# Performance work log

Hardware: AMD Instinct MI355X
Metric: run time of the kernel (lower is better)

## Reference

```python
import jax, jax.numpy as jnp
import numpy as np

EPS = 1e-12  # matches torch F.normalize default eps

def _l2_normalize(v, axis=-1):
    n = jnp.sqrt(jnp.sum(v * v, axis=axis, keepdims=True))
    return v / jnp.maximum(n, EPS)

def setup_inputs() -> dict:
    key = jax.random.key(0)
    k1, k2, k3 = jax.random.split(key, 3)
    B, S, D_IN, D_OUT, T = 4, 4096, 1024, 1024, 1024
    std = 1.0 / np.sqrt(D_IN)
    return {
        "x": jax.random.normal(k1, (B, S, D_IN), dtype=jnp.float32),
        "key_tokens": jax.random.normal(k2, (T, D_IN), dtype=jnp.float32) * std,
        "value_tokens": jax.random.normal(k3, (T, D_OUT), dtype=jnp.float32) * std,
        "temp": jnp.ones((T, 1), dtype=jnp.float32),
    }

def reference(x, key_tokens, value_tokens, temp):
    # x: [B,S,D_in]; key_tokens: [T,D_in]; value_tokens: [T,D_out]; temp: [T,1]
    x_norm = _l2_normalize(x)                      # [B,S,D_in]
    k_norm = _l2_normalize(key_tokens)             # [T,D_in]
    sim = jnp.einsum('bsd,td->bst', x_norm, k_norm)  # [B,S,T]
    sim = sim * jax.nn.sigmoid(temp).reshape(1, 1, -1)
    # mod_softmax: scale each row to RMS-norm sqrt(T), then exact GELU
    T = sim.shape[-1]
    scale = jnp.sqrt(jnp.float32(T)) / jnp.sqrt(jnp.sum(sim * sim, axis=-1, keepdims=True))
    weights = jax.nn.gelu(sim * scale, approximate=False)  # [B,S,T]
    return jnp.einsum('bst,to->bso', weights, value_tokens)  # [B,S,D_out]
```

## Files before the change

### kernel.cpp

```cpp
#include <hip/hip_runtime.h>
#include <math.h>

typedef __attribute__((ext_vector_type(8))) short short8;
typedef __attribute__((ext_vector_type(4))) float floatx4;

__device__ __forceinline__ float bf2f(unsigned short u) {
    union { unsigned int u; float f; } v;
    v.u = ((unsigned int)u) << 16;
    return v.f;
}

__device__ __forceinline__ unsigned short f2bf(float f) {
    union { float f; unsigned int u; } v;
    v.f = f;
    unsigned int r = v.u + 0x7fffu + ((v.u >> 16) & 1u);
    return (unsigned short)(r >> 16);
}

__device__ __forceinline__ void gload16_lds(const void* g, void* l) {
    __builtin_amdgcn_global_load_lds(
        (const __attribute__((address_space(1))) unsigned int*)g,
        (__attribute__((address_space(3))) unsigned int*)l, 16, 0, 0);
}

__device__ __forceinline__ ushort4 cvt4(float4 v, float fa) {
    ushort4 o;
    o.x = f2bf(v.x * fa); o.y = f2bf(v.y * fa);
    o.z = f2bf(v.z * fa); o.w = f2bf(v.w * fa);
    return o;
}

__global__ __launch_bounds__(256) void prep_kernel(
    const float* __restrict__ x, const float* __restrict__ key,
    const float* __restrict__ temp, const float* __restrict__ val,
    unsigned short* __restrict__ xb, unsigned short* __restrict__ kf,
    unsigned short* __restrict__ VT, float* __restrict__ rowsq,
    int M, int T, int D, int Dout, int nRowBlocks) {
    const int bid = blockIdx.x;
    if (bid < nRowBlocks) {
        const int lane = threadIdx.x & 63;
        const int nWaves = nRowBlocks << 2;
        const int totRows = M + T;
        for (int row = (bid << 2) | (int)(threadIdx.x >> 6); row < totRows;
             row += nWaves) {
            const bool isx = row < M;
            const int r = isx ? row : row - M;
            const float4* s4 =
                (const float4*)(isx ? (x + (size_t)r * D) : (key + (size_t)r * D));
            float4 v0 = s4[lane];
            float4 v1 = s4[lane + 64];
            float4 v2 = s4[lane + 128];
            float4 v3 = s4[lane + 192];
            float s = v0.x * v0.x + v0.y * v0.y + v0.z * v0.z + v0.w * v0.w;
            s += v1.x * v1.x + v1.y * v1.y + v1.z * v1.z + v1.w * v1.w;
            s += v2.x * v2.x + v2.y * v2.y + v2.z * v2.z + v2.w * v2.w;
            s += v3.x * v3.x + v3.y * v3.y + v3.z * v3.z + v3.w * v3.w;
#pragma unroll
            for (int o = 32; o > 0; o >>= 1) s += __shfl_xor(s, o, 64);
            float fa = 1.0f / fmaxf(sqrtf(s), 1e-12f);
            if (isx) {
                if (lane == 0) rowsq[r] = 0.0f;
            } else {
                fa = fa / (1.0f + expf(-temp[r]));
            }
            ushort4* dst =
                (ushort4*)(isx ? (xb + (size_t)r * D) : (kf + (size_t)r * D));
            dst[lane] = cvt4(v0, fa);
            dst[lane + 64] = cvt4(v1, fa);
            dst[lane + 128] = cvt4(v2, fa);
            dst[lane + 192] = cvt4(v3, fa);
        }
    } else {
        __shared__ unsigned short tile[64][65];
        const int idx = bid - nRowBlocks;
        const int nCt = Dout >> 6;
        const int c0 = (idx % nCt) * 64;
        const int r0 = (idx / nCt) * 64;
        const int t = threadIdx.x;
        for (int i = t; i < 4096; i += 256) {
            int rr = i >> 6, cc = i & 63;
            tile[rr][cc] = f2bf(val[(size_t)(r0 + rr) * Dout + c0 + cc]);
        }
        __syncthreads();
        for (int i = t; i < 4096; i += 256) {
            int rr = i >> 6, cc = i & 63;
            VT[(size_t)(c0 + rr) * T + r0 + cc] = tile[cc][rr];
        }
    }
}

template <int MODE>
__global__ __launch_bounds__(512, 2) void gemm256(
    const unsigned short* __restrict__ A, const unsigned short* __restrict__ B,
    void* __restrict__ Cv, float* __restrict__ rowsq, int M, int N, int K) {
    __shared__ __align__(16) char smem[131072];
    const int tid = threadIdx.x;
    const int lane = tid & 63;
    const int w = tid >> 6;
    const int wr = w >> 2;
    const int wc = w & 3;
    const int m0 = blockIdx.x * 256;
    const int n0 = blockIdx.y * 256;
    const int q = lane >> 4;
    const int cl = lane & 15;

    const int srow = lane >> 2;
    const int sch = (lane & 3) ^ ((lane & 32) >> 4);
    const unsigned short* gA0 = A + (size_t)(m0 + w * 16 + srow) * K + sch * 8;
    const unsigned short* gA1 = gA0 + (size_t)128 * K;
    const unsigned short* gB0 = B + (size_t)(n0 + w * 16 + srow) * K + sch * 8;
    const unsigned short* gB1 = gB0 + (size_t)128 * K;

    const int LB = (((lane & 15) * 64 + q * 16) ^ ((lane & 8) << 2));

    floatx4 acc[8][4];
#pragma unroll
    for (int i = 0; i < 8; i++)
#pragma unroll
        for (int j = 0; j < 4; j++) acc[i][j] = (floatx4){0.f, 0.f, 0.f, 0.f};

    const int NT = K >> 5;

    auto stage_h = [&](int t, int h) {
        char* base = smem + (size_t)(t & 3) * 32768 + (h * 8 + w) * 1024;
        const size_t ro = (size_t)h * 128 * K;
        const size_t ko = (size_t)t * 32;
        gload16_lds(gA0 + ro + ko, base);
        gload16_lds(gB0 + ro + ko, base + 16384);
    };
    (void)gA1; (void)gB1;

    stage_h(0, 0); stage_h(0, 1);
    stage_h(1, 0); stage_h(1, 1);
    stage_h(2, 0); stage_h(2, 1);
    asm volatile("s_waitcnt vmcnt(8)" ::: "memory");
    __builtin_amdgcn_s_barrier();

    for (int tt = 0; tt < NT; ++tt) {
        const char* sA = smem + (size_t)(tt & 3) * 32768;
        const char* sB = sA + 16384;
        const bool st = (tt + 3) < NT;
        short8 bf[4], af[4];
#pragma unroll
        for (int nt = 0; nt < 4; ++nt)
            bf[nt] = *(const short8*)(sB + (wc * 4 + nt) * 1024 + LB);
#pragma unroll
        for (int mt = 0; mt < 4; ++mt)
            af[mt] = *(const short8*)(sA + (wr * 8 + mt) * 1024 + LB);
        if (st) stage_h(tt + 3, 0);
        __builtin_amdgcn_s_barrier();
        asm volatile("s_waitcnt lgkmcnt(0)" ::: "memory");
        __builtin_amdgcn_s_setprio(1);
#pragma unroll
        for (int mt = 0; mt < 4; ++mt)
#pragma unroll
            for (int nt = 0; nt < 4; ++nt)
                acc[mt][nt] = __builtin_amdgcn_mfma_f32_16x16x32_bf16(
                    af[mt], bf[nt], acc[mt][nt], 0, 0, 0);
        __builtin_amdgcn_s_setprio(0);
        __builtin_amdgcn_s_barrier();
        __builtin_amdgcn_sched_barrier(0);
#pragma unroll
        for (int mt = 0; mt < 4; ++mt)
            af[mt] = *(const short8*)(sA + (wr * 8 + 4 + mt) * 1024 + LB);
        if (st) stage_h(tt + 3, 1);
        if (tt < NT - 3) {
            asm volatile("s_waitcnt vmcnt(8)" ::: "memory");
        } else if (tt == NT - 3) {
            asm volatile("s_waitcnt vmcnt(4)" ::: "memory");
        } else if (tt == NT - 2) {
            asm volatile("s_waitcnt vmcnt(0)" ::: "memory");
        }
        __builtin_amdgcn_s_barrier();
        asm volatile("s_waitcnt lgkmcnt(0)" ::: "memory");
        __builtin_amdgcn_s_setprio(1);
#pragma unroll
        for (int mt = 0; mt < 4; ++mt)
#pragma unroll
            for (int nt = 0; nt < 4; ++nt)
                acc[4 + mt][nt] = __builtin_amdgcn_mfma_f32_16x16x32_bf16(
                    af[mt], bf[nt], acc[4 + mt][nt], 0, 0, 0);
        __builtin_amdgcn_s_setprio(0);
        __builtin_amdgcn_s_barrier();
        __builtin_amdgcn_sched_barrier(0);
    }

#pragma unroll
    for (int mt = 0; mt < 8; ++mt) {
#pragma unroll
        for (int r = 0; r < 4; ++r) {
            const int m = m0 + wr * 128 + mt * 16 + q * 4 + r;
            if (MODE == 0) {
                unsigned short* C = (unsigned short*)Cv;
                float ssq = 0.f;
#pragma unroll
                for (int nt = 0; nt < 4; ++nt) {
                    float v = acc[mt][nt][r];
                    ssq += v * v;
                    C[(size_t)m * N + n0 + wc * 64 + nt * 16 + cl] = f2bf(v);
                }
#pragma unroll
                for (int o = 1; o < 16; o <<= 1) ssq += __shfl_xor(ssq, o, 64);
                if (cl == 0) atomicAdd(&rowsq[m], ssq);
            } else {
                float* C = (float*)Cv;
#pragma unroll
                for (int nt = 0; nt < 4; ++nt)
                    C[(size_t)m * N + n0 + wc * 64 + nt * 16 + cl] =
                        acc[mt][nt][r];
            }
        }
    }
}

__global__ __launch_bounds__(256) void gelu_kernel(unsigned short* __restrict__ sim,
                                                   const float* __restrict__ rowsq,
                                                   int nVec, int t8shift,
                                                   float sqrtT) {
    const int stride = gridDim.x * blockDim.x;
    const float kk = 0.70710678118654752f;
    for (int i = blockIdx.x * blockDim.x + threadIdx.x; i < nVec; i += stride) {
        short8 v = *(const short8*)(sim + (size_t)i * 8);
        const int row = i >> t8shift;
        const float scale = sqrtT / fmaxf(sqrtf(rowsq[row]), 1e-30f);
        short8 o;
#pragma unroll
        for (int j = 0; j < 8; j++) {
            float z = bf2f((unsigned short)v[j]) * scale;
            o[j] = (short)f2bf(0.5f * z * (1.0f + erff(z * kk)));
        }
        *(short8*)(sim + (size_t)i * 8) = o;
    }
}

extern "C" void kernel_launch(void* const* d_in, const int* in_sizes, int n_in,
                              void* d_out, int out_size, void* d_ws, size_t ws_size,
                              hipStream_t stream) {
    const float* x    = (const float*)d_in[0];
    const float* key  = (const float*)d_in[1];
    const float* val  = (const float*)d_in[2];
    const float* temp = (const float*)d_in[3];
    float* out = (float*)d_out;

    const int T = in_sizes[3];
    const int D = in_sizes[1] / T;
    const int Dout = in_sizes[2] / T;
    const int M = in_sizes[0] / D;

    char* ws = (char*)d_ws;
    size_t off = 0;
    unsigned short* xb  = (unsigned short*)(ws + off); off += (size_t)M * D * 2;
    unsigned short* sim = (unsigned short*)(ws + off); off += (size_t)M * T * 2;
    unsigned short* kf  = (unsigned short*)(ws + off); off += (size_t)T * D * 2;
    unsigned short* VT  = (unsigned short*)(ws + off); off += (size_t)Dout * T * 2;
    float* rowsq = (float*)(ws + off); off += (size_t)M * 4;
    (void)ws_size; (void)n_in; (void)out_size;

    const int nTrTiles = (T >> 6) * (Dout >> 6);
    const int nRowBlocks = 1024;
    prep_kernel<<<nRowBlocks + nTrTiles, 256, 0, stream>>>(
        x, key, temp, val, xb, kf, VT, rowsq, M, T, D, Dout, nRowBlocks);
    gemm256<0><<<dim3(M / 256, T / 256), 512, 0, stream>>>(xb, kf, sim, rowsq,
                                                           M, T, D);
    int t8shift = 0;
    {
        int t8 = T >> 3;
        while ((1 << t8shift) < t8) t8shift++;
    }
    gelu_kernel<<<2048, 256, 0, stream>>>(sim, rowsq, M * (T >> 3), t8shift,
                                          sqrtf((float)T));
    gemm256<1><<<dim3(M / 256, Dout / 256), 512, 0, stream>>>(sim, VT, out,
                                                              nullptr, M, Dout, T);
}
```

Baseline: 216.9 us.

## Shrink GEMM tiles to 256x128 with 4 waves and triple-buffered LDS

Both GEMMs switch from a 256x256 tile with 8 waves and a 4-stage LDS ring (128KB) to a 256x128 tile with 4 waves and a 3-stage ring (72KB). This doubles the grid (64x8 blocks) for better CU fill on M=16384 and cuts LDS per block so two blocks fit per CU. The price is lower data reuse per loaded byte, a shallower prefetch depth, and the removal of the sched_barriers, which frees the compiler to reorder around the MFMA phases.

```diff
diff --git a/kernel.cpp b/kernel.cpp
--- a/kernel.cpp
+++ b/kernel.cpp
@@ -90,28 +90,26 @@
 }
 
 template <int MODE>
-__global__ __launch_bounds__(512, 2) void gemm256(
+__global__ __launch_bounds__(256, 2) void gemm_pipe(
     const unsigned short* __restrict__ A, const unsigned short* __restrict__ B,
     void* __restrict__ Cv, float* __restrict__ rowsq, int M, int N, int K) {
-    __shared__ __align__(16) char smem[131072];
+    __shared__ __align__(16) char smem[73728];
     const int tid = threadIdx.x;
     const int lane = tid & 63;
     const int w = tid >> 6;
-    const int wr = w >> 2;
-    const int wc = w & 3;
+    const int wr = w >> 1;
+    const int wc = w & 1;
     const int m0 = blockIdx.x * 256;
-    const int n0 = blockIdx.y * 256;
+    const int n0 = blockIdx.y * 128;
     const int q = lane >> 4;
     const int cl = lane & 15;
 
     const int srow = lane >> 2;
     const int sch = (lane & 3) ^ ((lane & 32) >> 4);
-    const unsigned short* gA0 = A + (size_t)(m0 + w * 16 + srow) * K + sch * 8;
-    const unsigned short* gA1 = gA0 + (size_t)128 * K;
-    const unsigned short* gB0 = B + (size_t)(n0 + w * 16 + srow) * K + sch * 8;
-    const unsigned short* gB1 = gB0 + (size_t)128 * K;
-
-    const int LB = (((lane & 15) * 64 + q * 16) ^ ((lane & 8) << 2));
+    const unsigned short* gA = A + (size_t)(m0 + w * 16 + srow) * K + sch * 8;
+    const unsigned short* gB = B + (size_t)(n0 + w * 16 + srow) * K + sch * 8;
+
+    const int LB = ((cl * 64 + q * 16) ^ ((lane & 8) << 2));
 
     floatx4 acc[8][4];
 #pragma unroll
@@ -121,25 +119,26 @@
 
     const int NT = K >> 5;
 
-    auto stage_h = [&](int t, int h) {
-        char* base = smem + (size_t)(t & 3) * 32768 + (h * 8 + w) * 1024;
-        const size_t ro = (size_t)h * 128 * K;
-        const size_t ko = (size_t)t * 32;
-        gload16_lds(gA0 + ro + ko, base);
-        gload16_lds(gB0 + ro + ko, base + 16384);
+    auto stageA = [&](int t, int j) {
+        char* base = smem + (size_t)(t % 3) * 24576 + (w + 4 * j) * 1024;
+        gload16_lds(gA + (size_t)j * 64 * K + t * 32, base);
     };
-    (void)gA1; (void)gB1;
-
-    stage_h(0, 0); stage_h(0, 1);
-    stage_h(1, 0); stage_h(1, 1);
-    stage_h(2, 0); stage_h(2, 1);
-    asm volatile("s_waitcnt vmcnt(8)" ::: "memory");
+    auto stageB = [&](int t, int j) {
+        char* base = smem + (size_t)(t % 3) * 24576 + 16384 + (w + 4 * j) * 1024;
+        gload16_lds(gB + (size_t)j * 64 * K + t * 32, base);
+    };
+
+    stageA(0, 0); stageA(0, 1); stageB(0, 0);
+    stageA(0, 2); stageA(0, 3); stageB(0, 1);
+    stageA(1, 0); stageA(1, 1); stageB(1, 0);
+    stageA(1, 2); stageA(1, 3); stageB(1, 1);
+    asm volatile("s_waitcnt vmcnt(6)" ::: "memory");
     __builtin_amdgcn_s_barrier();
 
     for (int tt = 0; tt < NT; ++tt) {
-        const char* sA = smem + (size_t)(tt & 3) * 32768;
+        const char* sA = smem + (size_t)(tt % 3) * 24576;
         const char* sB = sA + 16384;
-        const bool st = (tt + 3) < NT;
+        const bool st = (tt + 2) < NT;
         short8 bf[4], af[4];
 #pragma unroll
         for (int nt = 0; nt < 4; ++nt)
@@ -147,7 +146,7 @@
 #pragma unroll
         for (int mt = 0; mt < 4; ++mt)
             af[mt] = *(const short8*)(sA + (wr * 8 + mt) * 1024 + LB);
-        if (st) stage_h(tt + 3, 0);
+        if (st) { stageA(tt + 2, 0); stageA(tt + 2, 1); stageB(tt + 2, 0); }
         __builtin_amdgcn_s_barrier();
         asm volatile("s_waitcnt lgkmcnt(0)" ::: "memory");
         __builtin_amdgcn_s_setprio(1);
@@ -159,15 +158,12 @@
                     af[mt], bf[nt], acc[mt][nt], 0, 0, 0);
         __builtin_amdgcn_s_setprio(0);
         __builtin_amdgcn_s_barrier();
-        __builtin_amdgcn_sched_barrier(0);
 #pragma unroll
         for (int mt = 0; mt < 4; ++mt)
             af[mt] = *(const short8*)(sA + (wr * 8 + 4 + mt) * 1024 + LB);
-        if (st) stage_h(tt + 3, 1);
-        if (tt < NT - 3) {
-            asm volatile("s_waitcnt vmcnt(8)" ::: "memory");
-        } else if (tt == NT - 3) {
-            asm volatile("s_waitcnt vmcnt(4)" ::: "memory");
+        if (st) { stageA(tt + 2, 2); stageA(tt + 2, 3); stageB(tt + 2, 1); }
+        if (st) {
+            asm volatile("s_waitcnt vmcnt(6)" ::: "memory");
         } else if (tt == NT - 2) {
             asm volatile("s_waitcnt vmcnt(0)" ::: "memory");
         }
@@ -182,7 +178,6 @@
                     af[mt], bf[nt], acc[4 + mt][nt], 0, 0, 0);
         __builtin_amdgcn_s_setprio(0);
         __builtin_amdgcn_s_barrier();
-        __builtin_amdgcn_sched_barrier(0);
     }
 
 #pragma unroll
@@ -260,8 +255,8 @@
     const int nRowBlocks = 1024;
     prep_kernel<<<nRowBlocks + nTrTiles, 256, 0, stream>>>(
         x, key, temp, val, xb, kf, VT, rowsq, M, T, D, Dout, nRowBlocks);
-    gemm256<0><<<dim3(M / 256, T / 256), 512, 0, stream>>>(xb, kf, sim, rowsq,
-                                                           M, T, D);
+    gemm_pipe<0><<<dim3(M / 256, T / 128), 256, 0, stream>>>(xb, kf, sim, rowsq,
+                                                             M, T, D);
     int t8shift = 0;
     {
         int t8 = T >> 3;
@@ -269,6 +264,6 @@
     }
     gelu_kernel<<<2048, 256, 0, stream>>>(sim, rowsq, M * (T >> 3), t8shift,
                                           sqrtf((float)T));
-    gemm256<1><<<dim3(M / 256, Dout / 256), 512, 0, stream>>>(sim, VT, out,
-                                                              nullptr, M, Dout, T);
-}
+    gemm_pipe<1><<<dim3(M / 256, Dout / 128), 256, 0, stream>>>(sim, VT, out,
+                                                                nullptr, M, Dout, T);
+}
```

Measured after the change: 218.8 us. No clear change (+0.9%).

## Pre-tile operands into MFMA fragment layout and load GEMM operands directly to registers

Applied to the files above, without the earlier changes.

The prep kernel now writes normalized x, keys and transposed values in a blocked 16x32 fragment layout, and the first GEMM writes sim in the same blocked layout. Both GEMMs then drop LDS staging and barriers, and each wave loads its MFMA fragments straight from global memory with register double-buffering. This removes LDS traffic and synchronisation. In exchange, data reuse across waves now depends on the L2/L1 caches instead of shared memory, so global load volume per block rises.

```diff
diff --git a/kernel.cpp b/kernel.cpp
--- a/kernel.cpp
+++ b/kernel.cpp
@@ -17,11 +17,6 @@
     return (unsigned short)(r >> 16);
 }
 
-__device__ __forceinline__ void gload16_lds(const void* g, void* l) {
-    __builtin_amdgcn_global_load_lds(
-        (const __attribute__((address_space(1))) unsigned int*)g,
-        (__attribute__((address_space(3))) unsigned int*)l, 16, 0, 0);
-}
 
 __device__ __forceinline__ ushort4 cvt4(float4 v, float fa) {
     ushort4 o;
@@ -63,12 +58,17 @@
             } else {
                 fa = fa / (1.0f + expf(-temp[r]));
             }
-            ushort4* dst =
-                (ushort4*)(isx ? (xb + (size_t)r * D) : (kf + (size_t)r * D));
-            dst[lane] = cvt4(v0, fa);
-            dst[lane + 64] = cvt4(v1, fa);
-            dst[lane + 128] = cvt4(v2, fa);
-            dst[lane + 192] = cvt4(v3, fa);
+            unsigned short* dst = isx ? xb : kf;
+            const int RT = (isx ? M : T) >> 4;
+            const size_t rb = (size_t)(r >> 4) * 512 + (r & 15) * 32;
+            float4 vv[4] = {v0, v1, v2, v3};
+#pragma unroll
+            for (int j = 0; j < 4; ++j) {
+                const int k0 = (lane + 64 * j) * 4;
+                const size_t ad =
+                    (size_t)(k0 >> 5) * RT * 512 + rb + (k0 & 31);
+                *(ushort4*)(dst + ad) = cvt4(vv[j], fa);
+            }
         }
     } else {
         __shared__ unsigned short tile[64][65];
@@ -77,6 +77,7 @@
         const int c0 = (idx % nCt) * 64;
         const int r0 = (idx / nCt) * 64;
         const int t = threadIdx.x;
+        const int DT = Dout >> 4;
         for (int i = t; i < 4096; i += 256) {
             int rr = i >> 6, cc = i & 63;
             tile[rr][cc] = f2bf(val[(size_t)(r0 + rr) * Dout + c0 + cc]);
@@ -84,16 +85,19 @@
         __syncthreads();
         for (int i = t; i < 4096; i += 256) {
             int rr = i >> 6, cc = i & 63;
-            VT[(size_t)(c0 + rr) * T + r0 + cc] = tile[cc][rr];
+            const int o = c0 + rr;
+            const int tt = r0 + cc;
+            const size_t ad = ((size_t)(tt >> 5) * DT + (o >> 4)) * 512 +
+                              (o & 15) * 32 + (tt & 31);
+            VT[ad] = tile[cc][rr];
         }
     }
 }
 
 template <int MODE>
-__global__ __launch_bounds__(512, 2) void gemm256(
+__global__ __launch_bounds__(512, 2) void gemm_direct(
     const unsigned short* __restrict__ A, const unsigned short* __restrict__ B,
     void* __restrict__ Cv, float* __restrict__ rowsq, int M, int N, int K) {
-    __shared__ __align__(16) char smem[131072];
     const int tid = threadIdx.x;
     const int lane = tid & 63;
     const int w = tid >> 6;
@@ -103,15 +107,17 @@
     const int n0 = blockIdx.y * 256;
     const int q = lane >> 4;
     const int cl = lane & 15;
-
-    const int srow = lane >> 2;
-    const int sch = (lane & 3) ^ ((lane & 32) >> 4);
-    const unsigned short* gA0 = A + (size_t)(m0 + w * 16 + srow) * K + sch * 8;
-    const unsigned short* gA1 = gA0 + (size_t)128 * K;
-    const unsigned short* gB0 = B + (size_t)(n0 + w * 16 + srow) * K + sch * 8;
-    const unsigned short* gB1 = gB0 + (size_t)128 * K;
-
-    const int LB = (((lane & 15) * 64 + q * 16) ^ ((lane & 8) << 2));
+    const int K32 = K >> 5;
+    const int Mt = M >> 4;
+    const int Nt = N >> 4;
+
+    const int laneoff = cl * 32 + q * 8;
+    const unsigned short* pA =
+        A + (size_t)((m0 >> 4) + wr * 8) * 512 + laneoff;
+    const unsigned short* pB =
+        B + (size_t)((n0 >> 4) + wc * 4) * 512 + laneoff;
+    const size_t sA = (size_t)Mt * 512;
+    const size_t sB = (size_t)Nt * 512;
 
     floatx4 acc[8][4];
 #pragma unroll
@@ -119,72 +125,36 @@
 #pragma unroll
         for (int j = 0; j < 4; j++) acc[i][j] = (floatx4){0.f, 0.f, 0.f, 0.f};
 
-    const int NT = K >> 5;
-
-    auto stage_h = [&](int t, int h) {
-        char* base = smem + (size_t)(t & 3) * 32768 + (h * 8 + w) * 1024;
-        const size_t ro = (size_t)h * 128 * K;
-        const size_t ko = (size_t)t * 32;
-        gload16_lds(gA0 + ro + ko, base);
-        gload16_lds(gB0 + ro + ko, base + 16384);
-    };
-    (void)gA1; (void)gB1;
-
-    stage_h(0, 0); stage_h(0, 1);
-    stage_h(1, 0); stage_h(1, 1);
-    stage_h(2, 0); stage_h(2, 1);
-    asm volatile("s_waitcnt vmcnt(8)" ::: "memory");
-    __builtin_amdgcn_s_barrier();
-
-    for (int tt = 0; tt < NT; ++tt) {
-        const char* sA = smem + (size_t)(tt & 3) * 32768;
-        const char* sB = sA + 16384;
-        const bool st = (tt + 3) < NT;
-        short8 bf[4], af[4];
-#pragma unroll
-        for (int nt = 0; nt < 4; ++nt)
-            bf[nt] = *(const short8*)(sB + (wc * 4 + nt) * 1024 + LB);
-#pragma unroll
-        for (int mt = 0; mt < 4; ++mt)
-            af[mt] = *(const short8*)(sA + (wr * 8 + mt) * 1024 + LB);
-        if (st) stage_h(tt + 3, 0);
-        __builtin_amdgcn_s_barrier();
-        asm volatile("s_waitcnt lgkmcnt(0)" ::: "memory");
-        __builtin_amdgcn_s_setprio(1);
-#pragma unroll
-        for (int mt = 0; mt < 4; ++mt)
-#pragma unroll
-            for (int nt = 0; nt < 4; ++nt)
-                acc[mt][nt] = __builtin_amdgcn_mfma_f32_16x16x32_bf16(
-                    af[mt], bf[nt], acc[mt][nt], 0, 0, 0);
-        __builtin_amdgcn_s_setprio(0);
-        __builtin_amdgcn_s_barrier();
-        __builtin_amdgcn_sched_barrier(0);
-#pragma unroll
-        for (int mt = 0; mt < 4; ++mt)
-            af[mt] = *(const short8*)(sA + (wr * 8 + 4 + mt) * 1024 + LB);
-        if (st) stage_h(tt + 3, 1);
-        if (tt < NT - 3) {
-            asm volatile("s_waitcnt vmcnt(8)" ::: "memory");
-        } else if (tt == NT - 3) {
-            asm volatile("s_waitcnt vmcnt(4)" ::: "memory");
-        } else if (tt == NT - 2) {
-            asm volatile("s_waitcnt vmcnt(0)" ::: "memory");
-        }
-        __builtin_amdgcn_s_barrier();
-        asm volatile("s_waitcnt lgkmcnt(0)" ::: "memory");
-        __builtin_amdgcn_s_setprio(1);
-#pragma unroll
-        for (int mt = 0; mt < 4; ++mt)
-#pragma unroll
-            for (int nt = 0; nt < 4; ++nt)
-                acc[4 + mt][nt] = __builtin_amdgcn_mfma_f32_16x16x32_bf16(
-                    af[mt], bf[nt], acc[4 + mt][nt], 0, 0, 0);
-        __builtin_amdgcn_s_setprio(0);
-        __builtin_amdgcn_s_barrier();
-        __builtin_amdgcn_sched_barrier(0);
-    }
-
+#define LOADS(AF, BF)                                                        \
+    _Pragma("unroll") for (int mt = 0; mt < 8; ++mt)                         \
+        AF[mt] = *(const short8*)(pA + mt * 512);                            \
+    _Pragma("unroll") for (int nt = 0; nt < 4; ++nt)                         \
+        BF[nt] = *(const short8*)(pB + nt * 512);                            \
+    pA += sA; pB += sB;
+
+#define STEP(AF, BF)                                                        \
+    _Pragma("unroll") for (int mt = 0; mt < 8; ++mt)                        \
+        _Pragma("unroll") for (int nt = 0; nt < 4; ++nt)                    \
+            acc[mt][nt] = __builtin_amdgcn_mfma_f32_16x16x32_bf16(          \
+                AF[mt], BF[nt], acc[mt][nt], 0, 0, 0);
+
+    short8 aA[8], bA[4], aB[8], bB[4];
+    LOADS(aA, bA)
+    int kt = 0;
+    for (; kt + 2 < K32; kt += 2) {
+        LOADS(aB, bB)
+        STEP(aA, bA)
+        LOADS(aA, bA)
+        STEP(aB, bB)
+    }
+    LOADS(aB, bB)
+    STEP(aA, bA)
+    STEP(aB, bB)
+#undef LOADS
+#undef STEP
+
+    const int mtb = (m0 >> 4) + wr * 8;
+    const int ntb = (n0 >> 5) + wc * 2;
 #pragma unroll
     for (int mt = 0; mt < 8; ++mt) {
 #pragma unroll
@@ -197,7 +167,10 @@
                 for (int nt = 0; nt < 4; ++nt) {
                     float v = acc[mt][nt][r];
                     ssq += v * v;
-                    C[(size_t)m * N + n0 + wc * 64 + nt * 16 + cl] = f2bf(v);
+                    const size_t ad =
+                        ((size_t)(ntb + (nt >> 1)) * Mt + (mtb + mt)) * 512 +
+                        (q * 4 + r) * 32 + (nt & 1) * 16 + cl;
+                    C[ad] = f2bf(v);
                 }
 #pragma unroll
                 for (int o = 1; o < 16; o <<= 1) ssq += __shfl_xor(ssq, o, 64);
@@ -215,13 +188,13 @@
 
 __global__ __launch_bounds__(256) void gelu_kernel(unsigned short* __restrict__ sim,
                                                    const float* __restrict__ rowsq,
-                                                   int nVec, int t8shift,
+                                                   int nVec, int MtMask,
                                                    float sqrtT) {
     const int stride = gridDim.x * blockDim.x;
     const float kk = 0.70710678118654752f;
     for (int i = blockIdx.x * blockDim.x + threadIdx.x; i < nVec; i += stride) {
         short8 v = *(const short8*)(sim + (size_t)i * 8);
-        const int row = i >> t8shift;
+        const int row = (((i >> 6) & MtMask) << 4) | ((i >> 2) & 15);
         const float scale = sqrtT / fmaxf(sqrtf(rowsq[row]), 1e-30f);
         short8 o;
 #pragma unroll
@@ -260,15 +233,10 @@
     const int nRowBlocks = 1024;
     prep_kernel<<<nRowBlocks + nTrTiles, 256, 0, stream>>>(
         x, key, temp, val, xb, kf, VT, rowsq, M, T, D, Dout, nRowBlocks);
-    gemm256<0><<<dim3(M / 256, T / 256), 512, 0, stream>>>(xb, kf, sim, rowsq,
-                                                           M, T, D);
-    int t8shift = 0;
-    {
-        int t8 = T >> 3;
-        while ((1 << t8shift) < t8) t8shift++;
-    }
-    gelu_kernel<<<2048, 256, 0, stream>>>(sim, rowsq, M * (T >> 3), t8shift,
+    gemm_direct<0><<<dim3(M / 256, T / 256), 512, 0, stream>>>(xb, kf, sim,
+                                                               rowsq, M, T, D);
+    gelu_kernel<<<2048, 256, 0, stream>>>(sim, rowsq, M * (T >> 3), (M >> 4) - 1,
                                           sqrtf((float)T));
-    gemm256<1><<<dim3(M / 256, Dout / 256), 512, 0, stream>>>(sim, VT, out,
-                                                              nullptr, M, Dout, T);
-}
+    gemm_direct<1><<<dim3(M / 256, Dout / 256), 512, 0, stream>>>(
+        sim, VT, out, nullptr, M, Dout, T);
+}
```

Result: slower. 246.6 us (+13.7%).

## Restructure GEMM main loop into 8-phase ping-pong pipeline with K=64 stages

Applied to the files above, without the earlier changes.

Replaces the 4-stage K=32 ring buffer GEMM loop with a two-buffer K=64 ping-pong schedule. Each tile is split into four MFMA quadrants, with LDS fragment reads and global-to-LDS loads interleaved between them, so memory traffic is meant to overlap with matrix-core work and fewer barriers are needed per unit of K. Shared memory moves to dynamic allocation of 128KB, set once through a function attribute. The hand-written vmcnt bookkeeping and prologue/epilogue tiles assume K is a multiple of 128, and getting them wrong risks races.

```diff
diff --git a/kernel.cpp b/kernel.cpp
--- a/kernel.cpp
+++ b/kernel.cpp
@@ -90,10 +90,10 @@
 }
 
 template <int MODE>
-__global__ __launch_bounds__(512, 2) void gemm256(
+__global__ __launch_bounds__(512, 2) void gemm8p(
     const unsigned short* __restrict__ A, const unsigned short* __restrict__ B,
     void* __restrict__ Cv, float* __restrict__ rowsq, int M, int N, int K) {
-    __shared__ __align__(16) char smem[131072];
+    extern __shared__ __align__(16) char smem[];
     const int tid = threadIdx.x;
     const int lane = tid & 63;
     const int w = tid >> 6;
@@ -106,12 +106,16 @@
 
     const int srow = lane >> 2;
     const int sch = (lane & 3) ^ ((lane & 32) >> 4);
-    const unsigned short* gA0 = A + (size_t)(m0 + w * 16 + srow) * K + sch * 8;
-    const unsigned short* gA1 = gA0 + (size_t)128 * K;
-    const unsigned short* gB0 = B + (size_t)(n0 + w * 16 + srow) * K + sch * 8;
-    const unsigned short* gB1 = gB0 + (size_t)128 * K;
-
-    const int LB = (((lane & 15) * 64 + q * 16) ^ ((lane & 8) << 2));
+    const unsigned short* rA0 = A + (size_t)(m0 + w * 16 + srow) * K + sch * 8;
+    const unsigned short* rA1 = rA0 + (size_t)128 * K;
+    const unsigned short* rB0 = B + (size_t)(n0 + w * 16 + srow) * K + sch * 8;
+    const unsigned short* rB1 = rB0 + (size_t)128 * K;
+
+    char* st = smem + w * 1024;
+
+    const int LB = ((cl * 64 + q * 16) ^ ((lane & 8) << 2));
+    const char* rd0 = (const char*)smem + LB;
+    const char* rd1 = rd0 + 65536;
 
     floatx4 acc[8][4];
 #pragma unroll
@@ -119,71 +123,111 @@
 #pragma unroll
         for (int j = 0; j < 4; j++) acc[i][j] = (floatx4){0.f, 0.f, 0.f, 0.f};
 
-    const int NT = K >> 5;
-
-    auto stage_h = [&](int t, int h) {
-        char* base = smem + (size_t)(t & 3) * 32768 + (h * 8 + w) * 1024;
-        const size_t ro = (size_t)h * 128 * K;
-        const size_t ko = (size_t)t * 32;
-        gload16_lds(gA0 + ro + ko, base);
-        gload16_lds(gB0 + ro + ko, base + 16384);
-    };
-    (void)gA1; (void)gB1;
-
-    stage_h(0, 0); stage_h(0, 1);
-    stage_h(1, 0); stage_h(1, 1);
-    stage_h(2, 0); stage_h(2, 1);
-    asm volatile("s_waitcnt vmcnt(8)" ::: "memory");
+    short8 a0[2][4], a1[2][4], b0[2][2], b1[2][2];
+
+#define RD_A(DST, RD, MSB)                                                   \
+    _Pragma("unroll") for (int ks = 0; ks < 2; ++ks)                         \
+        _Pragma("unroll") for (int mm = 0; mm < 4; ++mm)                     \
+            DST[ks][mm] = *(const short8*)(RD + ks * 16384 +                 \
+                                           (wr * 8 + MSB + mm) * 1024);
+
+#define RD_B(DST, RD, NSB)                                                   \
+    _Pragma("unroll") for (int ks = 0; ks < 2; ++ks)                         \
+        _Pragma("unroll") for (int nn = 0; nn < 2; ++nn)                     \
+            DST[ks][nn] = *(const short8*)(RD + 32768 + ks * 16384 +         \
+                                           (wc * 4 + NSB + nn) * 1024);
+
+#define MQ(MB, NB, AF, BFu)                                                  \
+    _Pragma("unroll") for (int ks = 0; ks < 2; ++ks)                         \
+        _Pragma("unroll") for (int mm = 0; mm < 4; ++mm)                     \
+            _Pragma("unroll") for (int nn = 0; nn < 2; ++nn)                 \
+                acc[MB + mm][NB + nn] =                                      \
+                    __builtin_amdgcn_mfma_f32_16x16x32_bf16(                 \
+                        AF[ks][mm], BFu[ks][nn], acc[MB + mm][NB + nn],      \
+                        0, 0, 0);
+
+#define LGKM0                                                                \
+    asm volatile("s_waitcnt lgkmcnt(0)" ::: "memory");                       \
+    __builtin_amdgcn_sched_barrier(0);
+
+#define VM4 asm volatile("s_waitcnt vmcnt(4)" ::: "memory");
+#define VM0 asm volatile("s_waitcnt vmcnt(0)" ::: "memory");
+
+#define TILE(RD, SBO, SBS, AEN, BEN, AOFF, BOFF, VMCODE)                     \
+    {                                                                        \
+        RD_A(a0, RD, 0)                                                      \
+        RD_B(b1, RD, 2)                                                      \
+        if (AEN) {                                                           \
+            gload16_lds(rA0 + (AOFF), st + (SBO));                           \
+            gload16_lds(rA0 + (AOFF) + 32, st + (SBO) + 16384);              \
+        }                                                                    \
+        LGKM0                                                                \
+        __builtin_amdgcn_s_setprio(1);                                       \
+        MQ(0, 2, a0, b1)                                                     \
+        __builtin_amdgcn_s_setprio(0);                                       \
+        __builtin_amdgcn_s_barrier();                                        \
+        RD_B(b0, RD, 0)                                                      \
+        if (AEN) {                                                           \
+            gload16_lds(rA1 + (AOFF), st + (SBO) + 8192);                    \
+            gload16_lds(rA1 + (AOFF) + 32, st + (SBO) + 24576);              \
+        }                                                                    \
+        LGKM0                                                                \
+        __builtin_amdgcn_s_setprio(1);                                       \
+        MQ(0, 0, a0, b0)                                                     \
+        __builtin_amdgcn_s_setprio(0);                                       \
+        __builtin_amdgcn_s_barrier();                                        \
+        RD_A(a1, RD, 4)                                                      \
+        if (BEN) {                                                           \
+            gload16_lds(rB0 + (BOFF), st + (SBS) + 32768);                   \
+            gload16_lds(rB0 + (BOFF) + 32, st + (SBS) + 49152);              \
+        }                                                                    \
+        LGKM0                                                                \
+        __builtin_amdgcn_s_setprio(1);                                       \
+        MQ(4, 0, a1, b0)                                                     \
+        __builtin_amdgcn_s_setprio(0);                                       \
+        __builtin_amdgcn_s_barrier();                                        \
+        if (BEN) {                                                           \
+            gload16_lds(rB1 + (BOFF), st + (SBS) + 40960);                   \
+            gload16_lds(rB1 + (BOFF) + 32, st + (SBS) + 57344);              \
+        }                                                                    \
+        __builtin_amdgcn_s_setprio(1);                                       \
+        MQ(4, 2, a1, b1)                                                     \
+        __builtin_amdgcn_s_setprio(0);                                       \
+        VMCODE                                                               \
+        __builtin_amdgcn_s_barrier();                                        \
+    }
+
+    gload16_lds(rB0, st + 32768);
+    gload16_lds(rB0 + 32, st + 49152);
+    gload16_lds(rB1, st + 40960);
+    gload16_lds(rB1 + 32, st + 57344);
+    gload16_lds(rA0, st);
+    gload16_lds(rA0 + 32, st + 16384);
+    gload16_lds(rA1, st + 8192);
+    gload16_lds(rA1 + 32, st + 24576);
+    gload16_lds(rB0 + 64, st + 65536 + 32768);
+    gload16_lds(rB0 + 96, st + 65536 + 49152);
+    gload16_lds(rB1 + 64, st + 65536 + 40960);
+    gload16_lds(rB1 + 96, st + 65536 + 57344);
+    VM4
     __builtin_amdgcn_s_barrier();
 
-    for (int tt = 0; tt < NT; ++tt) {
-        const char* sA = smem + (size_t)(tt & 3) * 32768;
-        const char* sB = sA + 16384;
-        const bool st = (tt + 3) < NT;
-        short8 bf[4], af[4];
-#pragma unroll
-        for (int nt = 0; nt < 4; ++nt)
-            bf[nt] = *(const short8*)(sB + (wc * 4 + nt) * 1024 + LB);
-#pragma unroll
-        for (int mt = 0; mt < 4; ++mt)
-            af[mt] = *(const short8*)(sA + (wr * 8 + mt) * 1024 + LB);
-        if (st) stage_h(tt + 3, 0);
-        __builtin_amdgcn_s_barrier();
-        asm volatile("s_waitcnt lgkmcnt(0)" ::: "memory");
-        __builtin_amdgcn_s_setprio(1);
-#pragma unroll
-        for (int mt = 0; mt < 4; ++mt)
-#pragma unroll
-            for (int nt = 0; nt < 4; ++nt)
-                acc[mt][nt] = __builtin_amdgcn_mfma_f32_16x16x32_bf16(
-                    af[mt], bf[nt], acc[mt][nt], 0, 0, 0);
-        __builtin_amdgcn_s_setprio(0);
-        __builtin_amdgcn_s_barrier();
-        __builtin_amdgcn_sched_barrier(0);
-#pragma unroll
-        for (int mt = 0; mt < 4; ++mt)
-            af[mt] = *(const short8*)(sA + (wr * 8 + 4 + mt) * 1024 + LB);
-        if (st) stage_h(tt + 3, 1);
-        if (tt < NT - 3) {
-            asm volatile("s_waitcnt vmcnt(8)" ::: "memory");
-        } else if (tt == NT - 3) {
-            asm volatile("s_waitcnt vmcnt(4)" ::: "memory");
-        } else if (tt == NT - 2) {
-            asm volatile("s_waitcnt vmcnt(0)" ::: "memory");
-        }
-        __builtin_amdgcn_s_barrier();
-        asm volatile("s_waitcnt lgkmcnt(0)" ::: "memory");
-        __builtin_amdgcn_s_setprio(1);
-#pragma unroll
-        for (int mt = 0; mt < 4; ++mt)
-#pragma unroll
-            for (int nt = 0; nt < 4; ++nt)
-                acc[4 + mt][nt] = __builtin_amdgcn_mfma_f32_16x16x32_bf16(
-                    af[mt], bf[nt], acc[4 + mt][nt], 0, 0, 0);
-        __builtin_amdgcn_s_setprio(0);
-        __builtin_amdgcn_s_barrier();
-        __builtin_amdgcn_sched_barrier(0);
-    }
+    const int NH = K >> 7;
+    for (int g = 0; g < NH - 1; ++g) {
+        TILE(rd0, 65536, 0, 1, 1, 64, 128, VM4)
+        TILE(rd1, 0, 65536, 1, 1, 128, 192, VM4)
+        rA0 += 128; rA1 += 128; rB0 += 128; rB1 += 128;
+    }
+    TILE(rd0, 65536, 0, 1, 0, 64, 0, VM0)
+    TILE(rd1, 0, 65536, 0, 0, 0, 0, )
+
+#undef TILE
+#undef RD_A
+#undef RD_B
+#undef MQ
+#undef LGKM0
+#undef VM4
+#undef VM0
 
 #pragma unroll
     for (int mt = 0; mt < 8; ++mt) {
@@ -256,12 +300,21 @@
     float* rowsq = (float*)(ws + off); off += (size_t)M * 4;
     (void)ws_size; (void)n_in; (void)out_size;
 
+    static bool s_attr = false;
+    if (!s_attr) {
+        hipFuncSetAttribute(reinterpret_cast<const void*>(&gemm8p<0>),
+                            hipFuncAttributeMaxDynamicSharedMemorySize, 131072);
+        hipFuncSetAttribute(reinterpret_cast<const void*>(&gemm8p<1>),
+                            hipFuncAttributeMaxDynamicSharedMemorySize, 131072);
+        s_attr = true;
+    }
+
     const int nTrTiles = (T >> 6) * (Dout >> 6);
     const int nRowBlocks = 1024;
     prep_kernel<<<nRowBlocks + nTrTiles, 256, 0, stream>>>(
         x, key, temp, val, xb, kf, VT, rowsq, M, T, D, Dout, nRowBlocks);
-    gemm256<0><<<dim3(M / 256, T / 256), 512, 0, stream>>>(xb, kf, sim, rowsq,
-                                                           M, T, D);
+    gemm8p<0><<<dim3(M / 256, T / 256), 512, 131072, stream>>>(xb, kf, sim,
+                                                               rowsq, M, T, D);
     int t8shift = 0;
     {
         int t8 = T >> 3;
@@ -269,6 +322,6 @@
     }
     gelu_kernel<<<2048, 256, 0, stream>>>(sim, rowsq, M * (T >> 3), t8shift,
                                           sqrtf((float)T));
-    gemm256<1><<<dim3(M / 256, Dout / 256), 512, 0, stream>>>(sim, VT, out,
-                                                              nullptr, M, Dout, T);
-}
+    gemm8p<1><<<dim3(M / 256, Dout / 256), 512, 131072, stream>>>(
+        sim, VT, out, nullptr, M, Dout, T);
+}
```

After: 208.2 us. 4.0% less time.
